# Optimization experiments

Hardware: AMD Instinct MI355X
Metric: run time of the kernel (lower is better)

Reference implementation:

```python
import jax, jax.numpy as jnp
import numpy as np

N = 50000    # nodes
E = 600000   # edges
F = 128      # num_features
ED = 16      # edge_dim
H = 4        # heads
D = 32       # per-head channels = hidden_units // heads
HID = H * D  # hidden_units = 128
C = 10       # num_classes


def _lin(k, fan_in, fan_out):
    # torch.nn.Linear-style init scale
    return jax.random.uniform(k, (fan_in, fan_out), jnp.float32, -1.0, 1.0) / np.sqrt(fan_in)


def setup_inputs() -> dict:
    key = jax.random.key(0)
    ks = jax.random.split(key, 24)
    inp = {
        "x": jax.random.normal(ks[0], (N, F), jnp.float32),
        "edge_index": jax.random.randint(ks[1], (2, E), 0, N, dtype=jnp.int32),
        "edge_attr": jax.random.normal(ks[2], (E, ED), jnp.float32),
    }
    j = 3
    for l, ind in enumerate([F, HID]):
        specs = {"q": (ind, HID, True), "k": (ind, HID, True), "v": (ind, HID, True),
                 "e": (ED, HID, False), "s": (ind, HID, True)}
        for nm, (i, o, bias) in specs.items():
            inp[f"W{nm}{l}"] = _lin(ks[j], i, o); j += 1
            if bias:
                inp[f"b{nm}{l}"] = jnp.zeros((o,), jnp.float32)
    inp["Wout"] = _lin(ks[j], HID, C)
    inp["bout"] = jnp.zeros((C,), jnp.float32)
    return inp


def _transformer_conv(x, src, dst, eattr, Wq, bq, Wk, bk, Wv, bv, We, Ws, bs):
    # PyG TransformerConv: concat=True, root_weight=True, beta=False, eval dropout.
    n = x.shape[0]
    q = (x @ Wq + bq).reshape(n, H, D)
    k = (x @ Wk + bk).reshape(n, H, D)
    v = (x @ Wv + bv).reshape(n, H, D)
    e = (eattr @ We).reshape(-1, H, D)           # edge embedding, added to key and value
    kj = k[src] + e                              # [E, H, D]
    vj = v[src] + e                              # [E, H, D]
    logits = jnp.einsum("ehd,ehd->eh", q[dst], kj) / np.sqrt(D)
    m = jax.ops.segment_max(logits, dst, num_segments=n)          # [N, H]
    ex = jnp.exp(logits - m[dst])
    denom = jax.ops.segment_sum(ex, dst, num_segments=n)          # [N, H]
    alpha = ex / (denom[dst] + 1e-16)                             # PyG softmax eps
    out = jax.ops.segment_sum(vj * alpha[..., None], dst, num_segments=n)
    return out.reshape(n, HID) + x @ Ws + bs                      # concat heads + skip


def reference(x, edge_index, edge_attr,
              Wq0, bq0, Wk0, bk0, Wv0, bv0, We0, Ws0, bs0,
              Wq1, bq1, Wk1, bk1, Wv1, bv1, We1, Ws1, bs1,
              Wout, bout):
    src, dst = edge_index[0], edge_index[1]
    h = jax.nn.relu(_transformer_conv(x, src, dst, edge_attr,
                                      Wq0, bq0, Wk0, bk0, Wv0, bv0, We0, Ws0, bs0))
    h = jax.nn.relu(_transformer_conv(h, src, dst, edge_attr,
                                      Wq1, bq1, Wk1, bk1, Wv1, bv1, We1, Ws1, bs1))
    logits = h @ Wout + bout
    return jax.nn.log_softmax(logits, axis=1)
```

## Files before the change

### kernel.cpp

```cpp
#include <hip/hip_runtime.h>

typedef unsigned short u16;
typedef unsigned int u32;
typedef __attribute__((ext_vector_type(4))) u16 u16x4;
typedef __attribute__((ext_vector_type(8))) u16 u16x8;
typedef __attribute__((ext_vector_type(4))) u32 u32x4;
typedef __attribute__((ext_vector_type(8))) short short8;
typedef __attribute__((ext_vector_type(4))) float f32x4;
typedef __attribute__((ext_vector_type(4))) float f4;
typedef __attribute__((ext_vector_type(2))) float f2;

#define NN 50000
#define NE 600000
#define HEADS 4
#define DH 32
#define HIDU 128
#define NC 10
#define NBLK 196
#define WES_T 34
#define WES_H 546

#define SCALE2 0.25503486164f

__device__ __forceinline__ float bf2f(u16 u) {
    union { unsigned int i; float f; } c; c.i = ((unsigned int)u) << 16; return c.f;
}
__device__ __forceinline__ u16 f2bf(float f) {
    union { float f; unsigned int i; } c; c.f = f;
    unsigned int x = c.i;
    return (u16)((x + 0x7fffu + ((x >> 16) & 1u)) >> 16);
}
__device__ __forceinline__ float lo_bf(u32 d) { return __uint_as_float(d << 16); }
__device__ __forceinline__ float hi_bf(u32 d) { return __uint_as_float(d & 0xffff0000u); }
__device__ __forceinline__ float qadd_xor1(float v) {
    int o = __builtin_amdgcn_update_dpp(0, __float_as_int(v), 0xB1, 0xF, 0xF, true);
    return v + __int_as_float(o);
}
__device__ __forceinline__ float qadd_xor2(float v) {
    int o = __builtin_amdgcn_update_dpp(0, __float_as_int(v), 0x4E, 0xF, 0xF, true);
    return v + __int_as_float(o);
}

__global__ void k_zero(int* p, int n) {
    int i = blockIdx.x * blockDim.x + threadIdx.x;
    if (i < n) p[i] = 0;
}

__global__ void k_hist(const int* __restrict__ dst, int* __restrict__ deg) {
    int i = blockIdx.x * blockDim.x + threadIdx.x;
    if (i < NE) atomicAdd(&deg[dst[i]], 1);
}

__global__ __launch_bounds__(256) void scan_a(const int* __restrict__ deg,
                                              int* __restrict__ bsum) {
    __shared__ int red[4];
    int i = blockIdx.x * 256 + threadIdx.x;
    int v = (i < NN) ? deg[i] : 0;
    #pragma unroll
    for (int off = 1; off < 64; off <<= 1) v += __shfl_xor(v, off);
    if ((threadIdx.x & 63) == 0) red[threadIdx.x >> 6] = v;
    __syncthreads();
    if (threadIdx.x == 0) bsum[blockIdx.x] = red[0] + red[1] + red[2] + red[3];
}

__global__ __launch_bounds__(256) void scan_b(const int* __restrict__ bsum,
                                              int* __restrict__ boff,
                                              int* __restrict__ row_ptr) {
    __shared__ int s[256];
    int t = threadIdx.x;
    int v = (t < NBLK) ? bsum[t] : 0;
    s[t] = v;
    __syncthreads();
    for (int off = 1; off < 256; off <<= 1) {
        int x = (t >= off) ? s[t - off] : 0;
        __syncthreads();
        s[t] += x;
        __syncthreads();
    }
    if (t < NBLK) boff[t] = s[t] - v;
    if (t == 0) row_ptr[NN] = NE;
}

__global__ __launch_bounds__(256) void scan_c(const int* __restrict__ deg,
                                              const int* __restrict__ boff,
                                              int* __restrict__ row_ptr,
                                              int* __restrict__ cursor) {
    __shared__ int s[256];
    int t = threadIdx.x;
    int i = blockIdx.x * 256 + t;
    int v = (i < NN) ? deg[i] : 0;
    s[t] = v;
    __syncthreads();
    for (int off = 1; off < 256; off <<= 1) {
        int x = (t >= off) ? s[t - off] : 0;
        __syncthreads();
        s[t] += x;
        __syncthreads();
    }
    if (i < NN) {
        int r = boff[blockIdx.x] + s[t] - v;
        row_ptr[i] = r;
        cursor[i] = r;
    }
}

__global__ void k_scatter(const int* __restrict__ ei, const float* __restrict__ eattr,
                          int* __restrict__ cursor,
                          int* __restrict__ csr_src, u16* __restrict__ ea16) {
    int i = blockIdx.x * blockDim.x + threadIdx.x;
    if (i < NE) {
        int s = ei[i];
        int d = ei[NE + i];
        int pos = atomicAdd(&cursor[d], 1);
        csr_src[pos] = s;
        const f4* ep = (const f4*)(eattr + (size_t)i * 16);
        f4 a = ep[0], b = ep[1], c = ep[2], dd = ep[3];
        u16x8 o0, o1;
        #pragma unroll
        for (int j = 0; j < 4; j++) {
            o0[j] = f2bf(a[j]); o0[4 + j] = f2bf(b[j]);
            o1[j] = f2bf(c[j]); o1[4 + j] = f2bf(dd[j]);
        }
        *(u16x8*)(ea16 + (size_t)pos * 16)     = o0;
        *(u16x8*)(ea16 + (size_t)pos * 16 + 8) = o1;
    }
}

__global__ void k_cvtw(const float* w0, const float* w1, const float* w2, const float* w3,
                       const float* w4, const float* w5, const float* w6, const float* w7,
                       u16* __restrict__ hi) {
    const float* w;
    switch (blockIdx.x) {
        case 0: w = w0; break; case 1: w = w1; break;
        case 2: w = w2; break; case 3: w = w3; break;
        case 4: w = w4; break; case 5: w = w5; break;
        case 6: w = w6; break; default: w = w7; break;
    }
    u16* oh = hi + blockIdx.x * 16384;
    #pragma unroll
    for (int i = 0; i < 8; i++) {
        int idx = threadIdx.x + (blockIdx.y * 8 + i) * 256;
        int k = idx >> 7, n = idx & 127;
        oh[n * 128 + k] = f2bf(w[idx]);
    }
}

__global__ __launch_bounds__(256) void gemm_qkvs(
    const float* __restrict__ X, const u16* __restrict__ WtHi,
    const float* __restrict__ b0, const float* __restrict__ b1,
    const float* __restrict__ b2, const float* __restrict__ b3,
    float* __restrict__ outq, u16* __restrict__ outk, u16* __restrict__ outv,
    float* __restrict__ outs, int nrows)
{
    __shared__ u16 Bs[128 * 128];
    const int mat = blockIdx.y;
    const u16* wh = WtHi + mat * 16384;

    #pragma unroll
    for (int i = 0; i < 8; i++) {
        int idx = threadIdx.x + i * 256;
        int n = idx >> 4, g = idx & 15;
        *(u16x8*)(&Bs[n * 128 + ((g ^ (n & 15)) << 3)]) = *(const u16x8*)(wh + n * 128 + g * 8);
    }
    __syncthreads();

    const int wave = threadIdx.x >> 6, lane = threadIdx.x & 63;
    const int n0 = lane & 15;
    const int qw = lane >> 4;
    const int kq = qw * 8;

    const float* xp[2];
    #pragma unroll
    for (int rt = 0; rt < 2; rt++) {
        int arow = blockIdx.x * 128 + wave * 32 + rt * 16 + n0;
        int arow_c = arow < nrows ? arow : nrows - 1;
        xp[rt] = X + (size_t)arow_c * HIDU + kq;
    }

    f32x4 acc[2][8];
    #pragma unroll
    for (int rt = 0; rt < 2; rt++)
        #pragma unroll
        for (int nt = 0; nt < 8; nt++) acc[rt][nt] = (f32x4){0.f, 0.f, 0.f, 0.f};

    #pragma unroll
    for (int ks = 0; ks < 4; ks++) {
        short8 ah[2];
        #pragma unroll
        for (int rt = 0; rt < 2; rt++) {
            f4 a0 = *(const f4*)(xp[rt] + ks * 32);
            f4 a1 = *(const f4*)(xp[rt] + ks * 32 + 4);
            #pragma unroll
            for (int j = 0; j < 4; j++) {
                ah[rt][j]     = (short)(__float_as_uint(a0[j]) >> 16);
                ah[rt][4 + j] = (short)(__float_as_uint(a1[j]) >> 16);
            }
        }
        #pragma unroll
        for (int nt = 0; nt < 8; nt++) {
            const int boff = (nt * 16 + n0) * 128 + (((ks << 2) + qw) ^ n0) * 8;
            short8 bh = *(const short8*)(&Bs[boff]);
            #pragma unroll
            for (int rt = 0; rt < 2; rt++)
                acc[rt][nt] = __builtin_amdgcn_mfma_f32_16x16x32_bf16(ah[rt], bh, acc[rt][nt], 0, 0, 0);
        }
    }

    const float* bia = (mat == 0) ? b0 : (mat == 1) ? b1 : (mat == 2) ? b2 : b3;
    #pragma unroll
    for (int rt = 0; rt < 2; rt++) {
        const int rbase = blockIdx.x * 128 + wave * 32 + rt * 16 + qw * 4;
        #pragma unroll
        for (int nt = 0; nt < 8; nt++) {
            int col = nt * 16 + n0;
            float bv = bia[col];
            #pragma unroll
            for (int r = 0; r < 4; r++) {
                int grow = rbase + r;
                if (grow < nrows) {
                    float v = acc[rt][nt][r] + bv;
                    if (mat == 0)      outq[(size_t)grow * HIDU + col] = v;
                    else if (mat == 1) outk[(size_t)grow * HIDU + col] = f2bf(v);
                    else if (mat == 2) outv[(size_t)grow * HIDU + col] = f2bf(v);
                    else               outs[(size_t)grow * HIDU + col] = v;
                }
            }
        }
    }
}

template<int MODE>
__global__ __launch_bounds__(256) void attn_t(
    const float* __restrict__ qb, const u16* __restrict__ kb, const u16* __restrict__ vb,
    const float* __restrict__ sb, const u16* __restrict__ ea16, const float* __restrict__ We,
    const int* __restrict__ row_ptr, const int* __restrict__ csr_src,
    float* __restrict__ hout_f32,
    const float* __restrict__ Wout, const float* __restrict__ bout,
    float* __restrict__ out_logits)
{
    __shared__ float WeS[4 * WES_H];
    __shared__ float WoT[MODE ? (NC * HIDU) : 1];
    __shared__ float boS[MODE ? NC : 1];

    #pragma unroll
    for (int i = 0; i < 8; i++) {
        int idx = threadIdx.x + i * 256;
        int tt = idx >> 7, c = idx & 127;
        int h = c >> 5, j = c & 31;
        WeS[h * WES_H + tt * WES_T + j] = We[idx];
    }
    if (MODE == 1) {
        #pragma unroll
        for (int i = 0; i < 5; i++) {
            int idx = threadIdx.x + i * 256;
            if (idx < HIDU * NC) {
                int c = idx >> 7, ch = idx & 127;
                WoT[idx] = Wout[ch * NC + c];
            }
        }
        if (threadIdx.x < NC) boS[threadIdx.x] = bout[threadIdx.x];
    }
    __syncthreads();

    int gtid = blockIdx.x * 256 + threadIdx.x;
    int n   = gtid >> 4;
    int l16 = gtid & 15;
    int h   = l16 >> 2;
    int sub = l16 & 3;
    const int lane = threadIdx.x & 63;
    const float* WeH = &WeS[h * WES_H];
    const int j0  = sub * 8;
    const int ch0 = h * DH + j0;
    const int t0  = sub * 4;

    f4 qa, qbv;
    {
        const f4* qp = (const f4*)(qb + (size_t)n * HIDU + ch0);
        qa = qp[0]; qbv = qp[1];
    }

    f4 g4v;
    {
        float part[16];
        #pragma unroll
        for (int t = 0; t < 16; t++) {
            const f2* wp = (const f2*)(WeH + t * WES_T + j0);
            f2 w0 = wp[0], w1 = wp[1], w2 = wp[2], w3 = wp[3];
            part[t] = qa[0] * w0.x + qa[1] * w0.y + qa[2] * w1.x + qa[3] * w1.y
                    + qbv[0] * w2.x + qbv[1] * w2.y + qbv[2] * w3.x + qbv[3] * w3.y;
        }
        #pragma unroll
        for (int t = 0; t < 16; t++) { part[t] = qadd_xor1(part[t]); part[t] = qadd_xor2(part[t]); }
        g4v[0] = part[t0]; g4v[1] = part[t0 + 1]; g4v[2] = part[t0 + 2]; g4v[3] = part[t0 + 3];
    }

    float l = 0.f;
    f4 O0 = {0.f, 0.f, 0.f, 0.f}, O1 = {0.f, 0.f, 0.f, 0.f};
    f4 a4 = {0.f, 0.f, 0.f, 0.f};

    const int r0 = row_ptr[n], r1 = row_ptr[n + 1];

    for (int e = r0; e < r1; e += 4) {
        const int e1 = (e + 1 < r1) ? e + 1 : e;
        const int e2 = (e + 2 < r1) ? e + 2 : e;
        const int e3 = (e + 3 < r1) ? e + 3 : e;
        int s0 = csr_src[e], s1 = csr_src[e1], s2 = csr_src[e2], s3 = csr_src[e3];
        u16x4 x0 = *(const u16x4*)(ea16 + (size_t)e  * 16 + t0);
        u16x4 x1 = *(const u16x4*)(ea16 + (size_t)e1 * 16 + t0);
        u16x4 x2 = *(const u16x4*)(ea16 + (size_t)e2 * 16 + t0);
        u16x4 x3 = *(const u16x4*)(ea16 + (size_t)e3 * 16 + t0);
        u32x4 k0 = *(const u32x4*)(kb + (size_t)s0 * HIDU + ch0);
        u32x4 k1 = *(const u32x4*)(kb + (size_t)s1 * HIDU + ch0);
        u32x4 k2 = *(const u32x4*)(kb + (size_t)s2 * HIDU + ch0);
        u32x4 k3 = *(const u32x4*)(kb + (size_t)s3 * HIDU + ch0);
        u32x4 v0 = *(const u32x4*)(vb + (size_t)s0 * HIDU + ch0);
        u32x4 v1 = *(const u32x4*)(vb + (size_t)s1 * HIDU + ch0);
        u32x4 v2 = *(const u32x4*)(vb + (size_t)s2 * HIDU + ch0);
        u32x4 v3 = *(const u32x4*)(vb + (size_t)s3 * HIDU + ch0);

        f4 ea0 = {bf2f(x0[0]), bf2f(x0[1]), bf2f(x0[2]), bf2f(x0[3])};
        f4 ea1 = {bf2f(x1[0]), bf2f(x1[1]), bf2f(x1[2]), bf2f(x1[3])};
        f4 ea2 = {bf2f(x2[0]), bf2f(x2[1]), bf2f(x2[2]), bf2f(x2[3])};
        f4 ea3 = {bf2f(x3[0]), bf2f(x3[1]), bf2f(x3[2]), bf2f(x3[3])};

        f4 ac0 = qa * (f4){lo_bf(k0[0]), hi_bf(k0[0]), lo_bf(k0[1]), hi_bf(k0[1])}
               + qbv * (f4){lo_bf(k0[2]), hi_bf(k0[2]), lo_bf(k0[3]), hi_bf(k0[3])}
               + g4v * ea0;
        f4 ac1 = qa * (f4){lo_bf(k1[0]), hi_bf(k1[0]), lo_bf(k1[1]), hi_bf(k1[1])}
               + qbv * (f4){lo_bf(k1[2]), hi_bf(k1[2]), lo_bf(k1[3]), hi_bf(k1[3])}
               + g4v * ea1;
        f4 ac2 = qa * (f4){lo_bf(k2[0]), hi_bf(k2[0]), lo_bf(k2[1]), hi_bf(k2[1])}
               + qbv * (f4){lo_bf(k2[2]), hi_bf(k2[2]), lo_bf(k2[3]), hi_bf(k2[3])}
               + g4v * ea2;
        f4 ac3 = qa * (f4){lo_bf(k3[0]), hi_bf(k3[0]), lo_bf(k3[1]), hi_bf(k3[1])}
               + qbv * (f4){lo_bf(k3[2]), hi_bf(k3[2]), lo_bf(k3[3]), hi_bf(k3[3])}
               + g4v * ea3;
        float d0 = (ac0[0] + ac0[1]) + (ac0[2] + ac0[3]);
        float d1 = (ac1[0] + ac1[1]) + (ac1[2] + ac1[3]);
        float d2 = (ac2[0] + ac2[1]) + (ac2[2] + ac2[3]);
        float d3 = (ac3[0] + ac3[1]) + (ac3[2] + ac3[3]);
        d0 = qadd_xor1(d0); d1 = qadd_xor1(d1); d2 = qadd_xor1(d2); d3 = qadd_xor1(d3);
        d0 = qadd_xor2(d0); d1 = qadd_xor2(d1); d2 = qadd_xor2(d2); d3 = qadd_xor2(d3);

        float w0 = exp2f(d0 * SCALE2);
        float w1 = (e + 1 < r1) ? exp2f(d1 * SCALE2) : 0.f;
        float w2 = (e + 2 < r1) ? exp2f(d2 * SCALE2) : 0.f;
        float w3 = (e + 3 < r1) ? exp2f(d3 * SCALE2) : 0.f;
        l += (w0 + w1) + (w2 + w3);

        O0 = O0
           + (f4){lo_bf(v0[0]), hi_bf(v0[0]), lo_bf(v0[1]), hi_bf(v0[1])} * w0
           + (f4){lo_bf(v1[0]), hi_bf(v1[0]), lo_bf(v1[1]), hi_bf(v1[1])} * w1
           + (f4){lo_bf(v2[0]), hi_bf(v2[0]), lo_bf(v2[1]), hi_bf(v2[1])} * w2
           + (f4){lo_bf(v3[0]), hi_bf(v3[0]), lo_bf(v3[1]), hi_bf(v3[1])} * w3;
        O1 = O1
           + (f4){lo_bf(v0[2]), hi_bf(v0[2]), lo_bf(v0[3]), hi_bf(v0[3])} * w0
           + (f4){lo_bf(v1[2]), hi_bf(v1[2]), lo_bf(v1[3]), hi_bf(v1[3])} * w1
           + (f4){lo_bf(v2[2]), hi_bf(v2[2]), lo_bf(v2[3]), hi_bf(v2[3])} * w2
           + (f4){lo_bf(v3[2]), hi_bf(v3[2]), lo_bf(v3[3]), hi_bf(v3[3])} * w3;
        a4 = a4 + ea0 * w0 + ea1 * w1 + ea2 * w2 + ea3 * w3;
    }

    float af[16];
    #pragma unroll
    for (int t = 0; t < 16; t++)
        af[t] = __shfl(a4[t & 3], (lane & ~3) | (t >> 2));

    float invl = 1.0f / (l + 1e-16f);
    const f4* sp = (const f4*)(sb + (size_t)n * HIDU + ch0);
    f4 sp0 = sp[0], sp1 = sp[1];

    f4 evA = {0.f, 0.f, 0.f, 0.f}, evB = {0.f, 0.f, 0.f, 0.f};
    #pragma unroll
    for (int t = 0; t < 16; t++) {
        float a = af[t];
        const f2* wp = (const f2*)(WeH + t * WES_T + j0);
        f2 w0 = wp[0], w1 = wp[1], w2 = wp[2], w3 = wp[3];
        evA[0] += a * w0.x; evA[1] += a * w0.y; evA[2] += a * w1.x; evA[3] += a * w1.y;
        evB[0] += a * w2.x; evB[1] += a * w2.y; evB[2] += a * w3.x; evB[3] += a * w3.y;
    }

    f4 val0, val1;
    #pragma unroll
    for (int j = 0; j < 4; j++) {
        val0[j] = fmaxf((O0[j] + evA[j]) * invl + sp0[j], 0.f);
        val1[j] = fmaxf((O1[j] + evB[j]) * invl + sp1[j], 0.f);
    }

    if (MODE == 0) {
        const size_t obase = (size_t)n * HIDU + ch0;
        *(f4*)(hout_f32 + obase) = val0;
        *(f4*)(hout_f32 + obase + 4) = val1;
    } else {
        float plg[NC];
        #pragma unroll
        for (int c = 0; c < NC; c++) {
            const f4* wr = (const f4*)(WoT + c * HIDU + ch0);
            f4 wa = wr[0], wb = wr[1];
            plg[c] = val0[0] * wa[0] + val0[1] * wa[1] + val0[2] * wa[2] + val0[3] * wa[3]
                   + val1[0] * wb[0] + val1[1] * wb[1] + val1[2] * wb[2] + val1[3] * wb[3];
        }
        #pragma unroll
        for (int mask = 1; mask < 16; mask <<= 1) {
            #pragma unroll
            for (int c = 0; c < NC; c++) plg[c] += __shfl_xor(plg[c], mask);
        }
        float lg[NC];
        float mx = -INFINITY;
        #pragma unroll
        for (int c = 0; c < NC; c++) { lg[c] = plg[c] + boS[c]; mx = fmaxf(mx, lg[c]); }
        float sum = 0.f;
        #pragma unroll
        for (int c = 0; c < NC; c++) sum += __expf(lg[c] - mx);
        float lse = mx + __logf(sum);
        if (l16 < NC) out_logits[(size_t)n * NC + l16] = lg[l16] - lse;
    }
}

extern "C" void kernel_launch(void* const* d_in, const int* in_sizes, int n_in,
                              void* d_out, int out_size, void* d_ws, size_t ws_size,
                              hipStream_t stream) {
    const float* x     = (const float*)d_in[0];
    const int*   ei    = (const int*)d_in[1];
    const float* eattr = (const float*)d_in[2];
    const float *Wq0 = (const float*)d_in[3],  *bq0 = (const float*)d_in[4];
    const float *Wk0 = (const float*)d_in[5],  *bk0 = (const float*)d_in[6];
    const float *Wv0 = (const float*)d_in[7],  *bv0 = (const float*)d_in[8];
    const float *We0 = (const float*)d_in[9];
    const float *Ws0 = (const float*)d_in[10], *bs0 = (const float*)d_in[11];
    const float *Wq1 = (const float*)d_in[12], *bq1 = (const float*)d_in[13];
    const float *Wk1 = (const float*)d_in[14], *bk1 = (const float*)d_in[15];
    const float *Wv1 = (const float*)d_in[16], *bv1 = (const float*)d_in[17];
    const float *We1 = (const float*)d_in[18];
    const float *Ws1 = (const float*)d_in[19], *bs1 = (const float*)d_in[20];
    const float *Wout = (const float*)d_in[21], *bout = (const float*)d_in[22];

    char* p = (char*)d_ws;
    auto alloc = [&](size_t bytes) -> void* {
        void* r = (void*)p;
        p += (bytes + 255) & ~(size_t)255;
        return r;
    };
    int* deg      = (int*)alloc(NN * 4);
    int* row_ptr  = (int*)alloc((NN + 1) * 4);
    int* cursor   = (int*)alloc(NN * 4);
    int* bsum     = (int*)alloc(NBLK * 4);
    int* boff     = (int*)alloc(NBLK * 4);
    int* csr_src  = (int*)alloc((size_t)NE * 4);
    float* qb     = (float*)alloc((size_t)NN * HIDU * 4);
    u16* kb       = (u16*)alloc((size_t)NN * HIDU * 2);
    u16* vb       = (u16*)alloc((size_t)NN * HIDU * 2);
    float* sbuf   = (float*)alloc((size_t)NN * HIDU * 4);
    float* hbuf   = (float*)alloc((size_t)NN * HIDU * 4);
    u16* ea16     = (u16*)alloc((size_t)NE * 16 * 2);
    u16* wthi     = (u16*)alloc(8 * 16384 * 2);

    k_zero<<<(NN + 255) / 256, 256, 0, stream>>>(deg, NN);
    k_hist<<<(NE + 255) / 256, 256, 0, stream>>>(ei + NE, deg);
    scan_a<<<NBLK, 256, 0, stream>>>(deg, bsum);
    scan_b<<<1, 256, 0, stream>>>(bsum, boff, row_ptr);
    scan_c<<<NBLK, 256, 0, stream>>>(deg, boff, row_ptr, cursor);
    k_scatter<<<(NE + 255) / 256, 256, 0, stream>>>(ei, eattr, cursor, csr_src, ea16);

    k_cvtw<<<dim3(8, 8), 256, 0, stream>>>(Wq0, Wk0, Wv0, Ws0, Wq1, Wk1, Wv1, Ws1, wthi);

    const int gm = (NN + 127) / 128;
    const int ga = (NN * 16) / 256;

    gemm_qkvs<<<dim3(gm, 4), 256, 0, stream>>>(x, wthi, bq0, bk0, bv0, bs0,
                                               qb, kb, vb, sbuf, NN);
    attn_t<0><<<ga, 256, 0, stream>>>(qb, kb, vb, sbuf, ea16, We0, row_ptr, csr_src,
                                      hbuf, nullptr, nullptr, nullptr);
    gemm_qkvs<<<dim3(gm, 4), 256, 0, stream>>>(hbuf, wthi + 4 * 16384, bq1, bk1, bv1, bs1,
                                               qb, kb, vb, sbuf, NN);
    attn_t<1><<<ga, 256, 0, stream>>>(qb, kb, vb, sbuf, ea16, We1, row_ptr, csr_src,
                                      nullptr, Wout, bout, (float*)d_out);
}
```

Measured before the change: 421.4 us.

## Sort destination nodes by in-degree to balance attention kernel workload

Builds a degree-bucketed permutation of nodes (histogram, scan, scatter) and has the attention kernels process nodes in that order, so each wavefront handles nodes with similar edge counts. This targets divergence and load imbalance from variable-length per-node edge loops. It adds three small kernels and an extra indirection, and node accesses to q/s/output become less sequential, which may hurt coalescing.

```diff
diff --git a/kernel.cpp b/kernel.cpp
--- a/kernel.cpp
+++ b/kernel.cpp
@@ -19,6 +19,7 @@
 #define NBLK 196
 #define WES_T 34
 #define WES_H 546
+#define DBINS 64
 
 #define SCALE2 0.25503486164f
 
@@ -104,6 +105,33 @@
     }
 }
 
+__global__ void k_dhist(const int* __restrict__ deg, int* __restrict__ dhist) {
+    int i = blockIdx.x * blockDim.x + threadIdx.x;
+    if (i < NN) atomicAdd(&dhist[min(deg[i], DBINS - 1)], 1);
+}
+
+__global__ __launch_bounds__(64) void k_dscan(const int* __restrict__ dhist,
+                                              int* __restrict__ dcur) {
+    int t = threadIdx.x;
+    int v = dhist[t];
+    int s = v;
+    #pragma unroll
+    for (int off = 1; off < 64; off <<= 1) {
+        int x = __shfl_up(s, off);
+        if (t >= off) s += x;
+    }
+    dcur[t] = s - v;
+}
+
+__global__ void k_dperm(const int* __restrict__ deg, int* __restrict__ dcur,
+                        int* __restrict__ perm) {
+    int i = blockIdx.x * blockDim.x + threadIdx.x;
+    if (i < NN) {
+        int pos = atomicAdd(&dcur[min(deg[i], DBINS - 1)], 1);
+        perm[pos] = i;
+    }
+}
+
 __global__ void k_scatter(const int* __restrict__ ei, const float* __restrict__ eattr,
                           int* __restrict__ cursor,
                           int* __restrict__ csr_src, u16* __restrict__ ea16) {
@@ -234,6 +262,7 @@
     const float* __restrict__ qb, const u16* __restrict__ kb, const u16* __restrict__ vb,
     const float* __restrict__ sb, const u16* __restrict__ ea16, const float* __restrict__ We,
     const int* __restrict__ row_ptr, const int* __restrict__ csr_src,
+    const int* __restrict__ perm,
     float* __restrict__ hout_f32,
     const float* __restrict__ Wout, const float* __restrict__ bout,
     float* __restrict__ out_logits)
@@ -263,7 +292,7 @@
     __syncthreads();
 
     int gtid = blockIdx.x * 256 + threadIdx.x;
-    int n   = gtid >> 4;
+    const int n = perm[gtid >> 4];
     int l16 = gtid & 15;
     int h   = l16 >> 2;
     int sub = l16 & 3;
@@ -441,11 +470,14 @@
         p += (bytes + 255) & ~(size_t)255;
         return r;
     };
-    int* deg      = (int*)alloc(NN * 4);
+    int* deg      = (int*)alloc((NN + 2 * DBINS) * 4);
+    int* dhist    = deg + NN;
+    int* dcur     = deg + NN + DBINS;
     int* row_ptr  = (int*)alloc((NN + 1) * 4);
     int* cursor   = (int*)alloc(NN * 4);
     int* bsum     = (int*)alloc(NBLK * 4);
     int* boff     = (int*)alloc(NBLK * 4);
+    int* perm     = (int*)alloc(NN * 4);
     int* csr_src  = (int*)alloc((size_t)NE * 4);
     float* qb     = (float*)alloc((size_t)NN * HIDU * 4);
     u16* kb       = (u16*)alloc((size_t)NN * HIDU * 2);
@@ -455,11 +487,14 @@
     u16* ea16     = (u16*)alloc((size_t)NE * 16 * 2);
     u16* wthi     = (u16*)alloc(8 * 16384 * 2);
 
-    k_zero<<<(NN + 255) / 256, 256, 0, stream>>>(deg, NN);
+    k_zero<<<(NN + 2 * DBINS + 255) / 256, 256, 0, stream>>>(deg, NN + 2 * DBINS);
     k_hist<<<(NE + 255) / 256, 256, 0, stream>>>(ei + NE, deg);
     scan_a<<<NBLK, 256, 0, stream>>>(deg, bsum);
     scan_b<<<1, 256, 0, stream>>>(bsum, boff, row_ptr);
     scan_c<<<NBLK, 256, 0, stream>>>(deg, boff, row_ptr, cursor);
+    k_dhist<<<NBLK, 256, 0, stream>>>(deg, dhist);
+    k_dscan<<<1, 64, 0, stream>>>(dhist, dcur);
+    k_dperm<<<NBLK, 256, 0, stream>>>(deg, dcur, perm);
     k_scatter<<<(NE + 255) / 256, 256, 0, stream>>>(ei, eattr, cursor, csr_src, ea16);
 
     k_cvtw<<<dim3(8, 8), 256, 0, stream>>>(Wq0, Wk0, Wv0, Ws0, Wq1, Wk1, Wv1, Ws1, wthi);
@@ -469,10 +504,10 @@
 
     gemm_qkvs<<<dim3(gm, 4), 256, 0, stream>>>(x, wthi, bq0, bk0, bv0, bs0,
                                                qb, kb, vb, sbuf, NN);
-    attn_t<0><<<ga, 256, 0, stream>>>(qb, kb, vb, sbuf, ea16, We0, row_ptr, csr_src,
+    attn_t<0><<<ga, 256, 0, stream>>>(qb, kb, vb, sbuf, ea16, We0, row_ptr, csr_src, perm,
                                       hbuf, nullptr, nullptr, nullptr);
     gemm_qkvs<<<dim3(gm, 4), 256, 0, stream>>>(hbuf, wthi + 4 * 16384, bq1, bk1, bv1, bs1,
                                                qb, kb, vb, sbuf, NN);
-    attn_t<1><<<ga, 256, 0, stream>>>(qb, kb, vb, sbuf, ea16, We1, row_ptr, csr_src,
+    attn_t<1><<<ga, 256, 0, stream>>>(qb, kb, vb, sbuf, ea16, We1, row_ptr, csr_src, perm,
                                       nullptr, Wout, bout, (float*)d_out);
 }
```

Result: slower. 732.9 us (+73.9%).
